# Kernel optimization log

Measured on AMD Instinct MI355X. Metric: run time of the kernel, lower is better.

## Reference

```python
import jax, jax.numpy as jnp
import numpy as np

N_NODES = 100000
N_GRAPHS = 64
EPS = 1e-5


def _sage_conv(x, src, dst, Wl, bl, Wr):
    # mean-aggregate neighbor messages (src -> dst), then lin_l(agg) + lin_r(x)
    n = x.shape[0]
    deg = jax.ops.segment_sum(jnp.ones_like(dst, dtype=x.dtype), dst, num_segments=n)
    agg = jax.ops.segment_sum(x[src], dst, num_segments=n)  # [N, d]
    agg = agg / jnp.maximum(deg, 1.0)[:, None]
    return agg @ Wl + bl + x @ Wr


def _bn_relu(x, gamma, beta):
    mu = jnp.mean(x, axis=0)
    var = jnp.var(x, axis=0)
    return jax.nn.relu((x - mu) * jax.lax.rsqrt(var + EPS) * gamma + beta)


def setup_inputs() -> dict:
    key = jax.random.key(0)
    ks = jax.random.split(key, 16)
    E = 1600000
    x = jax.random.normal(ks[0], (N_NODES, 2), dtype=jnp.float32)
    edge_index = jax.random.randint(ks[1], (2, E), 0, N_NODES, dtype=jnp.int64)
    batch = jnp.sort(jax.random.randint(ks[2], (N_NODES,), 0, N_GRAPHS, dtype=jnp.int64))

    def lin(k, din, dout):
        s = 1.0 / np.sqrt(din)
        return jax.random.uniform(k, (din, dout), jnp.float32, -s, s)

    d = {"x": x, "edge_index": edge_index, "batch": batch}
    dims = [(2, 32), (32, 64), (64, 128)]
    for i, (din, dout) in enumerate(dims, 1):
        k1, k2 = jax.random.split(ks[2 + i])
        d[f"Wl{i}"] = lin(k1, din, dout)
        d[f"bl{i}"] = jnp.zeros((dout,), jnp.float32)
        d[f"Wr{i}"] = lin(k2, din, dout)
        d[f"g{i}"] = jnp.ones((dout,), jnp.float32)
        d[f"be{i}"] = jnp.zeros((dout,), jnp.float32)
    d["Wf1"] = lin(ks[10], 128, 64)
    d["bf1"] = jnp.zeros((64,), jnp.float32)
    d["Wf2"] = lin(ks[11], 64, 1)
    d["bf2"] = jnp.zeros((1,), jnp.float32)
    return d


def reference(x, edge_index, batch,
              Wl1, bl1, Wr1, g1, be1,
              Wl2, bl2, Wr2, g2, be2,
              Wl3, bl3, Wr3, g3, be3,
              Wf1, bf1, Wf2, bf2):
    src, dst = edge_index[0], edge_index[1]
    h = _bn_relu(_sage_conv(x, src, dst, Wl1, bl1, Wr1), g1, be1)
    h = _bn_relu(_sage_conv(h, src, dst, Wl2, bl2, Wr2), g2, be2)
    h = _bn_relu(_sage_conv(h, src, dst, Wl3, bl3, Wr3), g3, be3)
    # global mean pool over graphs
    cnt = jax.ops.segment_sum(jnp.ones_like(batch, dtype=h.dtype), batch, num_segments=N_GRAPHS)
    pooled = jax.ops.segment_sum(h, batch, num_segments=N_GRAPHS) / jnp.maximum(cnt, 1.0)[:, None]
    out = jax.nn.relu(pooled @ Wf1 + bf1)
    # dropout is identity in eval mode
    return out @ Wf2 + bf2
```

## Files before the change

### kernel.cpp

```cpp
#include <hip/hip_runtime.h>
#include <hip/hip_fp16.h>

#define N_NODES 100000
#define N_GRAPHS 64
#define BN_EPS 1e-5

#define NB 782
#define NC 49
#define PT1 4096
#define PT2 2048
#define BPC 16
#define CAP 3072
#define CAPC 36864
#define CAPF 3072

typedef _Float16 f16x8 __attribute__((ext_vector_type(8)));
typedef float f32x4 __attribute__((ext_vector_type(4)));

union F16x8u {
    f16x8 v;
    __half2 h2[4];
    uint4 u;
};

__device__ __forceinline__ float bfly64(float v) {
#pragma unroll
    for (int m = 1; m < 64; m <<= 1) v += __shfl_xor(v, m, 64);
    return v;
}

__device__ __forceinline__ unsigned pack_h2(float a, float b) {
    __half2 h = __floats2half2_rn(a, b);
    unsigned w;
    __builtin_memcpy(&w, &h, 4);
    return w;
}

__device__ __forceinline__ float2 unpack_h2(unsigned w) {
    __half2 h;
    __builtin_memcpy(&h, &w, 4);
    return __half22float2(h);
}

__global__ void cur_init(int* __restrict__ ccur, int* __restrict__ fcur) {
    int t = threadIdx.x;
    if (t < NC) ccur[t] = t * CAPC;
    if (t < 784) fcur[t] = t * CAPF;
}

__global__ __launch_bounds__(256)
void part1(const int* __restrict__ dst, const int* __restrict__ src,
           int* __restrict__ ccur, int* __restrict__ cdst, int* __restrict__ csrc, int E) {
    __shared__ int ld[PT1], ls[PT1];
    __shared__ unsigned char lb[PT1];
    __shared__ int hist[NC], lbase[NC], gbase[NC];
    long long t0 = (long long)blockIdx.x * PT1;
    int n = (int)min((long long)PT1, (long long)E - t0);
    int tid = threadIdx.x;
    for (int i = tid; i < NC; i += 256) hist[i] = 0;
    __syncthreads();
    int d[PT1 / 256], s[PT1 / 256], c[PT1 / 256];
#pragma unroll
    for (int k = 0; k < PT1 / 256; ++k) {
        int li = k * 256 + tid;
        if (li < n) {
            d[k] = __builtin_nontemporal_load(dst + t0 + li);
            s[k] = __builtin_nontemporal_load(src + t0 + li);
            c[k] = d[k] >> 11;
            atomicAdd(&hist[c[k]], 1);
        }
    }
    __syncthreads();
    if (tid == 0) {
        int run = 0;
        for (int i = 0; i < NC; ++i) { lbase[i] = run; run += hist[i]; }
    }
    __syncthreads();
    if (tid < NC) gbase[tid] = atomicAdd(&ccur[tid], hist[tid]);
    __syncthreads();
    for (int i = tid; i < NC; i += 256) hist[i] = 0;
    __syncthreads();
#pragma unroll
    for (int k = 0; k < PT1 / 256; ++k) {
        int li = k * 256 + tid;
        if (li < n) {
            int pos = lbase[c[k]] + atomicAdd(&hist[c[k]], 1);
            ld[pos] = d[k]; ls[pos] = s[k]; lb[pos] = (unsigned char)c[k];
        }
    }
    __syncthreads();
    for (int i = tid; i < n; i += 256) {
        int bb = lb[i];
        int g = gbase[bb] + (i - lbase[bb]);
        cdst[g] = ld[i];
        csrc[g] = ls[i];
    }
}

__global__ __launch_bounds__(256)
void part2(const int* __restrict__ cdst, const int* __restrict__ csrc,
           const int* __restrict__ ccur, int* __restrict__ fcur,
           int* __restrict__ qdst, int* __restrict__ qsrc) {
    __shared__ int ld[PT2], ls[PT2];
    __shared__ unsigned char lb[PT2];
    __shared__ int hist[16], lbase[16], gbase[16];
    int c = blockIdx.x / BPC;
    int j = blockIdx.x % BPC;
    int beg = c * CAPC;
    int end = ccur[c];
    int tid = threadIdx.x;
    for (int t0 = beg + j * PT2; t0 < end; t0 += BPC * PT2) {
        int n = min(PT2, end - t0);
        if (tid < 16) hist[tid] = 0;
        __syncthreads();
        int d[PT2 / 256], s[PT2 / 256], f[PT2 / 256];
#pragma unroll
        for (int k = 0; k < PT2 / 256; ++k) {
            int li = k * 256 + tid;
            if (li < n) {
                d[k] = cdst[t0 + li];
                s[k] = csrc[t0 + li];
                f[k] = (d[k] >> 7) & 15;
                atomicAdd(&hist[f[k]], 1);
            }
        }
        __syncthreads();
        if (tid == 0) {
            int run = 0;
            for (int i = 0; i < 16; ++i) { lbase[i] = run; run += hist[i]; }
        }
        __syncthreads();
        if (tid < 16) gbase[tid] = atomicAdd(&fcur[(c << 4) + tid], hist[tid]);
        __syncthreads();
        if (tid < 16) hist[tid] = 0;
        __syncthreads();
#pragma unroll
        for (int k = 0; k < PT2 / 256; ++k) {
            int li = k * 256 + tid;
            if (li < n) {
                int pos = lbase[f[k]] + atomicAdd(&hist[f[k]], 1);
                ld[pos] = d[k]; ls[pos] = s[k]; lb[pos] = (unsigned char)f[k];
            }
        }
        __syncthreads();
        for (int i = tid; i < n; i += 256) {
            int bb = lb[i];
            int g = gbase[bb] + (i - lbase[bb]);
            qdst[g] = ld[i];
            qsrc[g] = ls[i];
        }
        __syncthreads();
    }
}

__global__ __launch_bounds__(256)
void fill_final(const int* __restrict__ qdst, const int* __restrict__ qsrc,
                const int* __restrict__ fcur, int* __restrict__ offs,
                int* __restrict__ oend, int* __restrict__ nbr, int N) {
    __shared__ int cnt[128], cbase[128], cur[128];
    __shared__ int lout[CAP];
    int b = blockIdx.x;
    int nlo = b << 7;
    int nn = min(128, N - nlo);
    int ebeg = b * CAPF;
    int ne = fcur[b] - ebeg;
    int tid = threadIdx.x;
    if (tid < 128) { cnt[tid] = 0; cur[tid] = 0; }
    __syncthreads();
    for (int i = tid; i < ne; i += 256)
        atomicAdd(&cnt[qdst[ebeg + i] - nlo], 1);
    __syncthreads();
    if (tid < 128) cbase[tid] = cnt[tid];
    __syncthreads();
    for (int st = 1; st < 128; st <<= 1) {
        int v = 0;
        if (tid < 128 && tid >= st) v = cbase[tid - st];
        __syncthreads();
        if (tid < 128 && tid >= st) cbase[tid] += v;
        __syncthreads();
    }
    if (tid < nn) {
        offs[nlo + tid] = ebeg + (tid ? cbase[tid - 1] : 0);
        oend[nlo + tid] = ebeg + cbase[tid];
    }
    __syncthreads();
    for (int i = tid; i < ne; i += 256) {
        int d = qdst[ebeg + i];
        int s = qsrc[ebeg + i];
        int ln = d - nlo;
        int p = (ln ? cbase[ln - 1] : 0) + atomicAdd(&cur[ln], 1);
        lout[p] = s;
    }
    __syncthreads();
    for (int i = tid; i < ne; i += 256)
        nbr[ebeg + i] = lout[i];
}

__global__ __launch_bounds__(256)
void layer1_fused(const float2* __restrict__ x2,
                  const int* __restrict__ offs, const int* __restrict__ oend,
                  const int* __restrict__ nbr,
                  const float* __restrict__ Wl, const float* __restrict__ bl,
                  const float* __restrict__ Wr,
                  __half* __restrict__ hout16,
                  double* __restrict__ sums, int N) {
    __shared__ float sAr[64];
    int tid = threadIdx.x;
    if (tid < 64) sAr[tid] = 0.f;
    __syncthreads();
    int n = blockIdx.x * 256 + tid;
    bool valid = (n < N);
    int beg = 0, end = 0;
    if (valid) { beg = offs[n]; end = oend[n]; }
    float ax0 = 0.f, ay0 = 0.f, ax1 = 0.f, ay1 = 0.f;
    int j = beg;
    for (; j + 16 <= end; j += 16) {
        int s[16];
#pragma unroll
        for (int u = 0; u < 16; ++u) s[u] = __builtin_nontemporal_load(nbr + j + u);
        float2 v[16];
#pragma unroll
        for (int u = 0; u < 16; ++u) v[u] = x2[s[u]];
#pragma unroll
        for (int u = 0; u < 16; ++u) {
            if (u & 1) { ax1 += v[u].x; ay1 += v[u].y; }
            else       { ax0 += v[u].x; ay0 += v[u].y; }
        }
    }
    for (; j + 4 <= end; j += 4) {
        int s[4];
#pragma unroll
        for (int u = 0; u < 4; ++u) s[u] = __builtin_nontemporal_load(nbr + j + u);
        float2 v[4];
#pragma unroll
        for (int u = 0; u < 4; ++u) v[u] = x2[s[u]];
        ax0 += v[0].x; ay0 += v[0].y;
        ax1 += v[1].x; ay1 += v[1].y;
        ax0 += v[2].x; ay0 += v[2].y;
        ax1 += v[3].x; ay1 += v[3].y;
    }
    for (; j < end; ++j) {
        float2 v = x2[nbr[j]];
        ax0 += v.x; ay0 += v.y;
    }
    float invd = 1.0f / fmaxf((float)(end - beg), 1.0f);
    float a0 = (ax0 + ax1) * invd, a1 = (ay0 + ay1) * invd;
    float x0 = 0.f, x1 = 0.f;
    if (valid) {
        float2 xv = x2[n];
        x0 = xv.x; x1 = xv.y;
    }
    float acc[32];
#pragma unroll
    for (int jj = 0; jj < 32; ++jj)
        acc[jj] = bl[jj] + a0 * Wl[jj] + a1 * Wl[32 + jj] + x0 * Wr[jj] + x1 * Wr[32 + jj];
    if (valid) {
        unsigned w[16];
#pragma unroll
        for (int p = 0; p < 16; ++p) w[p] = pack_h2(acc[2*p], acc[2*p+1]);
        uint4* q = (uint4*)(hout16 + (size_t)n * 32);
        q[0] = make_uint4(w[0], w[1], w[2], w[3]);
        q[1] = make_uint4(w[4], w[5], w[6], w[7]);
        q[2] = make_uint4(w[8], w[9], w[10], w[11]);
        q[3] = make_uint4(w[12], w[13], w[14], w[15]);
    }
    int lane = tid & 63;
#pragma unroll
    for (int jj = 0; jj < 32; ++jj) {
        float v = valid ? acc[jj] : 0.f;
        float s = bfly64(v);
        float q = bfly64(v * v);
        if (lane == jj) atomicAdd(&sAr[jj], s);
        if (lane == 32 + jj) atomicAdd(&sAr[32 + jj], q);
    }
    __syncthreads();
    if (tid < 64) atomicAdd(&sums[tid], (double)sAr[tid]);
}

template<int F>
__global__ __launch_bounds__(256)
void bn_apply(const uint4* __restrict__ h, const double* __restrict__ sums,
              const float* __restrict__ gamma, const float* __restrict__ beta,
              uint4* __restrict__ out, int N) {
    __shared__ __align__(16) float lsc[F], lsf[F];
    int tid = threadIdx.x;
    if (tid < F) {
        double mu = sums[tid] / (double)N_NODES;
        double var = sums[F + tid] / (double)N_NODES - mu * mu;
        if (var < 0.0) var = 0.0;
        double sc = (double)gamma[tid] / sqrt(var + BN_EPS);
        lsc[tid] = (float)sc;
        lsf[tid] = (float)((double)beta[tid] - mu * sc);
    }
    __syncthreads();
    constexpr int FV = F / 8;
    int total = N * FV;
    for (int i = blockIdx.x * 256 + tid; i < total; i += gridDim.x * 256) {
        uint4 v = h[i];
        int c4 = (i & (FV - 1)) * 2;
        float4 sca = ((const float4*)lsc)[c4];
        float4 scb = ((const float4*)lsc)[c4 + 1];
        float4 sfa = ((const float4*)lsf)[c4];
        float4 sfb = ((const float4*)lsf)[c4 + 1];
        float2 f0 = unpack_h2(v.x), f1 = unpack_h2(v.y);
        float2 f2 = unpack_h2(v.z), f3 = unpack_h2(v.w);
        uint4 o;
        o.x = pack_h2(fmaxf(f0.x * sca.x + sfa.x, 0.f), fmaxf(f0.y * sca.y + sfa.y, 0.f));
        o.y = pack_h2(fmaxf(f1.x * sca.z + sfa.z, 0.f), fmaxf(f1.y * sca.w + sfa.w, 0.f));
        o.z = pack_h2(fmaxf(f2.x * scb.x + sfb.x, 0.f), fmaxf(f2.y * scb.y + sfb.y, 0.f));
        o.w = pack_h2(fmaxf(f3.x * scb.z + sfb.z, 0.f), fmaxf(f3.y * scb.w + sfb.w, 0.f));
        out[i] = o;
    }
}

__device__ __forceinline__ void accum8_h16(float* acc, uint4 v) {
    float2 f0 = unpack_h2(v.x), f1 = unpack_h2(v.y);
    float2 f2 = unpack_h2(v.z), f3 = unpack_h2(v.w);
    acc[0] += f0.x; acc[1] += f0.y; acc[2] += f1.x; acc[3] += f1.y;
    acc[4] += f2.x; acc[5] += f2.y; acc[6] += f3.x; acc[7] += f3.y;
}

template<int F>
__global__ __launch_bounds__(256)
void agg_sum(const uint4* __restrict__ xb, const int* __restrict__ offs,
             const int* __restrict__ oend, const int* __restrict__ nbr,
             uint4* __restrict__ aggh, int N) {
    constexpr int FV = F / 8;
    constexpr int NPB = 256 / FV;
    int n = blockIdx.x * NPB + threadIdx.y;
    if (n >= N) return;
    int f = threadIdx.x;
    int beg = offs[n], end = oend[n];
    float a0[8], a1[8];
#pragma unroll
    for (int q = 0; q < 8; ++q) { a0[q] = 0.f; a1[q] = 0.f; }
    int j = beg;
    for (; j + 16 <= end; j += 16) {
        int s[16];
#pragma unroll
        for (int u = 0; u < 16; ++u) s[u] = __builtin_nontemporal_load(nbr + j + u);
        uint4 v[16];
#pragma unroll
        for (int u = 0; u < 16; ++u) v[u] = xb[s[u] * FV + f];
#pragma unroll
        for (int u = 0; u < 16; ++u)
            accum8_h16((u & 1) ? a1 : a0, v[u]);
    }
    if (j + 8 <= end) {
        int s[8];
#pragma unroll
        for (int u = 0; u < 8; ++u) s[u] = __builtin_nontemporal_load(nbr + j + u);
        uint4 v[8];
#pragma unroll
        for (int u = 0; u < 8; ++u) v[u] = xb[s[u] * FV + f];
#pragma unroll
        for (int u = 0; u < 8; ++u)
            accum8_h16((u & 1) ? a1 : a0, v[u]);
        j += 8;
    }
    if (j + 4 <= end) {
        int s[4];
#pragma unroll
        for (int u = 0; u < 4; ++u) s[u] = __builtin_nontemporal_load(nbr + j + u);
        uint4 v[4];
#pragma unroll
        for (int u = 0; u < 4; ++u) v[u] = xb[s[u] * FV + f];
#pragma unroll
        for (int u = 0; u < 4; ++u)
            accum8_h16((u & 1) ? a1 : a0, v[u]);
        j += 4;
    }
    for (; j < end; ++j) {
        uint4 v = xb[__builtin_nontemporal_load(nbr + j) * FV + f];
        accum8_h16(a0, v);
    }
    float invd = 1.0f / fmaxf((float)(end - beg), 1.0f);
    uint4 o;
    o.x = pack_h2((a0[0] + a1[0]) * invd, (a0[1] + a1[1]) * invd);
    o.y = pack_h2((a0[2] + a1[2]) * invd, (a0[3] + a1[3]) * invd);
    o.z = pack_h2((a0[4] + a1[4]) * invd, (a0[5] + a1[5]) * invd);
    o.w = pack_h2((a0[6] + a1[6]) * invd, (a0[7] + a1[7]) * invd);
    aggh[n * FV + f] = o;
}

__global__ __launch_bounds__(256)
void pack_w(const float* __restrict__ Wl2, const float* __restrict__ Wr2,
            const float* __restrict__ Wl3, const float* __restrict__ Wr3,
            __half* __restrict__ pk) {
    int e = blockIdx.x * 256 + threadIdx.x;
    const float* W; int le, DOUT, NCB, base, SZ;
    if (e < 2048)       { W = Wl2; le = e;         DOUT = 64;  NCB = 4; base = 0;     SZ = 2048; }
    else if (e < 4096)  { W = Wr2; le = e - 2048;  DOUT = 64;  NCB = 4; base = 4096;  SZ = 2048; }
    else if (e < 12288) { W = Wl3; le = e - 4096;  DOUT = 128; NCB = 8; base = 8192;  SZ = 8192; }
    else                { W = Wr3; le = e - 12288; DOUT = 128; NCB = 8; base = 24576; SZ = 8192; }
    int i = le & 7;
    int lane = (le >> 3) & 63;
    int cbkb = le >> 9;
    int cb = cbkb % NCB;
    int kb = cbkb / NCB;
    int k = kb * 32 + ((lane >> 4) << 3) + i;
    int col = cb * 16 + (lane & 15);
    float w = W[k * DOUT + col];
    __half h = __float2half(w);
    float lo = w - __half2float(h);
    pk[base + le] = h;
    pk[base + SZ + le] = __float2half(lo);
}

template<int DIN, int DOUT>
__global__ __launch_bounds__(256)
void linear_mfma(const __half* __restrict__ bnx16, const __half* __restrict__ agg16,
                 const __half* __restrict__ wlhi, const __half* __restrict__ wllo,
                 const __half* __restrict__ wrhi, const __half* __restrict__ wrlo,
                 const float* __restrict__ bl,
                 __half* __restrict__ hout16, float* __restrict__ partial, int N) {
    constexpr int KB = DIN / 32;
    constexpr int NCB = DOUT / 16;
    constexpr int MREP = 2;
    constexpr int MB = 4 * MREP * 16;
    __shared__ float blkS[DOUT], blkQ[DOUT];
    int tid = threadIdx.x;
    for (int i = tid; i < DOUT; i += 256) { blkS[i] = 0.f; blkQ[i] = 0.f; }
    __syncthreads();
    int n0 = blockIdx.x * MB;

    int wave = tid >> 6;
    int lane = tid & 63;
    int rlane = lane & 15;
    int kg = lane >> 4;
    int rbase = n0 + wave * (MREP * 16);

    f16x8 aA[MREP][KB], aX[MREP][KB];
#pragma unroll
    for (int m = 0; m < MREP; ++m) {
        int row = rbase + m * 16 + rlane;
        int rowc = min(row, N - 1);
#pragma unroll
        for (int kb = 0; kb < KB; ++kb) {
            int c0 = kb * 32 + kg * 8;
            F16x8u ta, tx;
            ta.u = *(const uint4*)(agg16 + (size_t)rowc * DIN + c0);
            tx.u = *(const uint4*)(bnx16 + (size_t)rowc * DIN + c0);
            aA[m][kb] = ta.v;
            aX[m][kb] = tx.v;
        }
    }

    f32x4 acc[MREP][NCB];
#pragma unroll
    for (int cb = 0; cb < NCB; ++cb) {
        float bv = bl[cb * 16 + rlane];
#pragma unroll
        for (int m = 0; m < MREP; ++m)
            acc[m][cb] = {bv, bv, bv, bv};
    }

#pragma unroll
    for (int cb = 0; cb < NCB; ++cb) {
#pragma unroll
        for (int kb = 0; kb < KB; ++kb) {
            size_t fo = ((size_t)(kb * NCB + cb) * 64 + lane) * 8;
            f16x8 blh = *(const f16x8*)(wlhi + fo);
            f16x8 bll = *(const f16x8*)(wllo + fo);
            f16x8 brh = *(const f16x8*)(wrhi + fo);
            f16x8 brl = *(const f16x8*)(wrlo + fo);
#pragma unroll
            for (int m = 0; m < MREP; ++m) {
                acc[m][cb] = __builtin_amdgcn_mfma_f32_16x16x32_f16(aA[m][kb], blh, acc[m][cb], 0, 0, 0);
                acc[m][cb] = __builtin_amdgcn_mfma_f32_16x16x32_f16(aA[m][kb], bll, acc[m][cb], 0, 0, 0);
                acc[m][cb] = __builtin_amdgcn_mfma_f32_16x16x32_f16(aX[m][kb], brh, acc[m][cb], 0, 0, 0);
                acc[m][cb] = __builtin_amdgcn_mfma_f32_16x16x32_f16(aX[m][kb], brl, acc[m][cb], 0, 0, 0);
            }
        }
    }

#pragma unroll
    for (int m = 0; m < MREP; ++m) {
        int rowb = rbase + m * 16 + kg * 4;
#pragma unroll
        for (int r = 0; r < 4; ++r) {
            int node = rowb + r;
            if (node < N) {
#pragma unroll
                for (int cb = 0; cb < NCB; ++cb)
                    hout16[(size_t)node * DOUT + cb * 16 + rlane] = __float2half(acc[m][cb][r]);
            }
        }
    }

#pragma unroll
    for (int cb = 0; cb < NCB; ++cb) {
        float s = 0.f, q = 0.f;
#pragma unroll
        for (int m = 0; m < MREP; ++m) {
            int rowb = rbase + m * 16 + kg * 4;
#pragma unroll
            for (int r = 0; r < 4; ++r) {
                if (rowb + r < N) {
                    float v = acc[m][cb][r];
                    s += v; q += v * v;
                }
            }
        }
        s += __shfl_xor(s, 16, 64); s += __shfl_xor(s, 32, 64);
        q += __shfl_xor(q, 16, 64); q += __shfl_xor(q, 32, 64);
        if (kg == 0) {
            atomicAdd(&blkS[cb * 16 + rlane], s);
            atomicAdd(&blkQ[cb * 16 + rlane], q);
        }
    }
    __syncthreads();
    float* po = partial + (size_t)blockIdx.x * (2 * DOUT);
    for (int i = tid; i < DOUT; i += 256) {
        po[i] = blkS[i];
        po[DOUT + i] = blkQ[i];
    }
}

template<int F>
__global__ __launch_bounds__(256)
void stats_finalize2(const float* __restrict__ partial, double* __restrict__ sums, int P) {
    __shared__ double sh[256];
    int i = blockIdx.x;
    int t = threadIdx.x;
    double a = 0.0;
    for (int k = t; k < P; k += 256)
        a += (double)partial[(size_t)k * (2 * F) + i];
    sh[t] = a;
    __syncthreads();
    for (int st = 128; st > 0; st >>= 1) {
        if (t < st) sh[t] += sh[t + st];
        __syncthreads();
    }
    if (t == 0) sums[i] = sh[0];
}

__global__ void pool_partial(const __half* __restrict__ h, const int* __restrict__ batch,
                             const double* __restrict__ sums,
                             const float* __restrict__ gamma, const float* __restrict__ beta,
                             double* __restrict__ pooled_d, int N) {
    __shared__ float lsc[128], lsf[128];
    const int CH = 64;
    int f = threadIdx.x;
    {
        double mu = sums[f] / (double)N_NODES;
        double var = sums[128 + f] / (double)N_NODES - mu * mu;
        if (var < 0.0) var = 0.0;
        double sc = (double)gamma[f] / sqrt(var + BN_EPS);
        lsc[f] = (float)sc;
        lsf[f] = (float)((double)beta[f] - mu * sc);
    }
    __syncthreads();
    int n0 = blockIdx.x * CH;
    if (n0 >= N) return;
    int n1 = min(n0 + CH, N);
    float sc = lsc[f], sf = lsf[f];
    int g = batch[n0];
    float acc = 0.f;
    for (int n = n0; n < n1; ++n) {
        int bg = batch[n];
        if (bg != g) {
            atomicAdd(&pooled_d[g * 128 + f], (double)acc);
            acc = 0.f;
            g = bg;
        }
        float v = __half2float(h[(long long)n * 128 + f]);
        acc += fmaxf(v * sc + sf, 0.f);
    }
    atomicAdd(&pooled_d[g * 128 + f], (double)acc);
}

__global__ void mlp_fused(const double* __restrict__ pooled_d, const int* __restrict__ batch,
                          const float* __restrict__ Wf1, const float* __restrict__ bf1,
                          const float* __restrict__ Wf2, const float* __restrict__ bf2,
                          float* __restrict__ out, int N) {
    __shared__ float sp[128];
    int g = blockIdx.x;
    int t = threadIdx.x;
    int lo = 0, hi = N;
    while (lo < hi) { int m = (lo + hi) >> 1; if (batch[m] < g) lo = m + 1; else hi = m; }
    int start = lo;
    hi = N;
    while (lo < hi) { int m = (lo + hi) >> 1; if (batch[m] < g + 1) lo = m + 1; else hi = m; }
    int cnt = lo - start;
    sp[t] = (float)(pooled_d[g * 128 + t] / (double)max(cnt, 1));
    __syncthreads();
    if (t < 64) {
        float hacc = bf1[t];
#pragma unroll 8
        for (int k = 0; k < 128; ++k) hacc += sp[k] * Wf1[k * 64 + t];
        hacc = fmaxf(hacc, 0.f) * Wf2[t];
        for (int o = 32; o > 0; o >>= 1) hacc += __shfl_down(hacc, o);
        if (t == 0) out[g] = hacc + bf2[0];
    }
}

extern "C" void kernel_launch(void* const* d_in, const int* in_sizes, int n_in,
                              void* d_out, int out_size, void* d_ws, size_t ws_size,
                              hipStream_t stream) {
    const float* x     = (const float*)d_in[0];
    const int*   ei    = (const int*)d_in[1];
    const int*   batch = (const int*)d_in[2];
    const float *Wl1=(const float*)d_in[3],  *bl1=(const float*)d_in[4],  *Wr1=(const float*)d_in[5];
    const float *g1 =(const float*)d_in[6],  *be1=(const float*)d_in[7];
    const float *Wl2=(const float*)d_in[8],  *bl2=(const float*)d_in[9],  *Wr2=(const float*)d_in[10];
    const float *g2 =(const float*)d_in[11], *be2=(const float*)d_in[12];
    const float *Wl3=(const float*)d_in[13], *bl3=(const float*)d_in[14], *Wr3=(const float*)d_in[15];
    const float *g3 =(const float*)d_in[16], *be3=(const float*)d_in[17];
    const float *Wf1=(const float*)d_in[18], *bf1=(const float*)d_in[19];
    const float *Wf2=(const float*)d_in[20], *bf2=(const float*)d_in[21];

    const int N = N_NODES;
    const int E = in_sizes[1] / 2;
    const int* src = ei;
    const int* dst = ei + E;

    char* ws = (char*)d_ws;
    size_t off = 0;
    auto salloc = [&](size_t bytes) {
        void* p = ws + off;
        off += (bytes + 255) & ~(size_t)255;
        return p;
    };
    double* sums    = (double*)salloc(768 * 8);
    double* pooledd = (double*)salloc((size_t)N_GRAPHS * 128 * 8);
    size_t zero_bytes = off;
    int*    offs    = (int*)   salloc((size_t)N * 4);
    int*    oend    = (int*)   salloc((size_t)N * 4);
    int*    fcur    = (int*)   salloc(784 * 4);
    int*    ccur    = (int*)   salloc(NC * 4);
    int*    nbr     = (int*)   salloc((size_t)NB * CAPF * 4);
    float*  partial = (float*) salloc((size_t)1024 * 256 * 4);
    __half* pk      = (__half*)salloc((size_t)40960 * 2);
    __half* h1h     = (__half*)salloc((size_t)(N + 256) * 32 * 2);
    __half* b1h     = (__half*)salloc((size_t)(N + 256) * 32 * 2);
    __half* h2h     = (__half*)salloc((size_t)(N + 256) * 64 * 2);
    __half* b2h     = (__half*)salloc((size_t)(N + 256) * 64 * 2);
    __half* h3h     = (__half*)salloc((size_t)(N + 256) * 128 * 2);
    __half* aggh    = (__half*)salloc((size_t)(N + 256) * 64 * 2);
    (void)ws_size;

    double* sums1 = sums, *sums2 = sums + 256, *sums3 = sums + 512;
    int* cdst = (int*)h3h;
    int* csrc = cdst + (size_t)NC * CAPC;
    int* qdst = (int*)aggh;
    int* qsrc = (int*)h2h;

    const __half *pwl2h = pk,         *pwl2l = pk + 2048;
    const __half *pwr2h = pk + 4096,  *pwr2l = pk + 6144;
    const __half *pwl3h = pk + 8192,  *pwl3l = pk + 16384;
    const __half *pwr3h = pk + 24576, *pwr3l = pk + 32768;

    hipMemsetAsync(sums, 0, zero_bytes, stream);

    pack_w<<<80, 256, 0, stream>>>(Wl2, Wr2, Wl3, Wr3, pk);
    cur_init<<<1, 1024, 0, stream>>>(ccur, fcur);

    part1<<<(E + PT1 - 1) / PT1, 256, 0, stream>>>(dst, src, ccur, cdst, csrc, E);
    part2<<<NC * BPC, 256, 0, stream>>>(cdst, csrc, ccur, fcur, qdst, qsrc);
    fill_final<<<NB, 256, 0, stream>>>(qdst, qsrc, fcur, offs, oend, nbr, N);

    const int NL = (N + 255) / 256;
    const int NBLK = (N + 127) / 128;

    layer1_fused<<<NL, 256, 0, stream>>>((const float2*)x, offs, oend, nbr,
                                          Wl1, bl1, Wr1, h1h, sums1, N);

    bn_apply<32><<<512, 256, 0, stream>>>((const uint4*)h1h, sums1, g1, be1, (uint4*)b1h, N);
    agg_sum<32><<<(N + 63) / 64, dim3(4, 64), 0, stream>>>(
        (const uint4*)b1h, offs, oend, nbr, (uint4*)aggh, N);
    linear_mfma<32, 64><<<NBLK, 256, 0, stream>>>(
        b1h, (const __half*)aggh, pwl2h, pwl2l, pwr2h, pwr2l, bl2, h2h, partial, N);
    stats_finalize2<64><<<128, 256, 0, stream>>>(partial, sums2, NBLK);

    bn_apply<64><<<512, 256, 0, stream>>>((const uint4*)h2h, sums2, g2, be2, (uint4*)b2h, N);
    agg_sum<64><<<(N + 31) / 32, dim3(8, 32), 0, stream>>>(
        (const uint4*)b2h, offs, oend, nbr, (uint4*)aggh, N);
    linear_mfma<64, 128><<<NBLK, 256, 0, stream>>>(
        b2h, (const __half*)aggh, pwl3h, pwl3l, pwr3h, pwr3l, bl3, h3h, partial, N);
    stats_finalize2<128><<<256, 256, 0, stream>>>(partial, sums3, NBLK);

    pool_partial<<<(N + 63) / 64, 128, 0, stream>>>(h3h, batch, sums3, g3, be3, pooledd, N);
    mlp_fused<<<N_GRAPHS, 128, 0, stream>>>(pooledd, batch, Wf1, bf1, Wf2, bf2, (float*)d_out, N);
}
```

Before: 312.4 us.

## Pack dst low bits and src into one int for edge partition passes

After: 307.4 us. Within noise of the previous version (-1.6%).

```diff
diff --git a/kernel.cpp b/kernel.cpp
--- a/kernel.cpp
+++ b/kernel.cpp
@@ -42,16 +42,40 @@
     return __half22float2(h);
 }
 
-__global__ void cur_init(int* __restrict__ ccur, int* __restrict__ fcur) {
-    int t = threadIdx.x;
-    if (t < NC) ccur[t] = t * CAPC;
-    if (t < 784) fcur[t] = t * CAPF;
-}
+__global__ __launch_bounds__(256)
+void pack_w(const float* __restrict__ Wl2, const float* __restrict__ Wr2,
+            const float* __restrict__ Wl3, const float* __restrict__ Wr3,
+            __half* __restrict__ pk, int* __restrict__ ccur, int* __restrict__ fcur) {
+    int tid = threadIdx.x;
+    if (blockIdx.x == 0) {
+        for (int t = tid; t < NC; t += 256) ccur[t] = t * CAPC;
+        for (int t = tid; t < 784; t += 256) fcur[t] = t * CAPF;
+    }
+    int e = blockIdx.x * 256 + tid;
+    const float* W; int le, DOUT, NCB, base, SZ;
+    if (e < 2048)       { W = Wl2; le = e;         DOUT = 64;  NCB = 4; base = 0;     SZ = 2048; }
+    else if (e < 4096)  { W = Wr2; le = e - 2048;  DOUT = 64;  NCB = 4; base = 4096;  SZ = 2048; }
+    else if (e < 12288) { W = Wl3; le = e - 4096;  DOUT = 128; NCB = 8; base = 8192;  SZ = 8192; }
+    else                { W = Wr3; le = e - 12288; DOUT = 128; NCB = 8; base = 24576; SZ = 8192; }
+    int i = le & 7;
+    int lane = (le >> 3) & 63;
+    int cbkb = le >> 9;
+    int cb = cbkb % NCB;
+    int kb = cbkb / NCB;
+    int k = kb * 32 + ((lane >> 4) << 3) + i;
+    int col = cb * 16 + (lane & 15);
+    float w = W[k * DOUT + col];
+    __half h = __float2half(w);
+    float lo = w - __half2float(h);
+    pk[base + le] = h;
+    pk[base + SZ + le] = __float2half(lo);
+}
+
 
 __global__ __launch_bounds__(256)
 void part1(const int* __restrict__ dst, const int* __restrict__ src,
-           int* __restrict__ ccur, int* __restrict__ cdst, int* __restrict__ csrc, int E) {
-    __shared__ int ld[PT1], ls[PT1];
+           int* __restrict__ ccur, int* __restrict__ cpk, int E) {
+    __shared__ int ld[PT1];
     __shared__ unsigned char lb[PT1];
     __shared__ int hist[NC], lbase[NC], gbase[NC];
     long long t0 = (long long)blockIdx.x * PT1;
@@ -59,14 +83,15 @@
     int tid = threadIdx.x;
     for (int i = tid; i < NC; i += 256) hist[i] = 0;
     __syncthreads();
-    int d[PT1 / 256], s[PT1 / 256], c[PT1 / 256];
+    int p[PT1 / 256], c[PT1 / 256];
 #pragma unroll
     for (int k = 0; k < PT1 / 256; ++k) {
         int li = k * 256 + tid;
         if (li < n) {
-            d[k] = __builtin_nontemporal_load(dst + t0 + li);
-            s[k] = __builtin_nontemporal_load(src + t0 + li);
-            c[k] = d[k] >> 11;
+            int d = __builtin_nontemporal_load(dst + t0 + li);
+            int s = __builtin_nontemporal_load(src + t0 + li);
+            c[k] = d >> 11;
+            p[k] = ((d & 2047) << 17) | s;
             atomicAdd(&hist[c[k]], 1);
         }
     }
@@ -85,23 +110,21 @@
         int li = k * 256 + tid;
         if (li < n) {
             int pos = lbase[c[k]] + atomicAdd(&hist[c[k]], 1);
-            ld[pos] = d[k]; ls[pos] = s[k]; lb[pos] = (unsigned char)c[k];
+            ld[pos] = p[k]; lb[pos] = (unsigned char)c[k];
         }
     }
     __syncthreads();
     for (int i = tid; i < n; i += 256) {
         int bb = lb[i];
         int g = gbase[bb] + (i - lbase[bb]);
-        cdst[g] = ld[i];
-        csrc[g] = ls[i];
-    }
-}
-
-__global__ __launch_bounds__(256)
-void part2(const int* __restrict__ cdst, const int* __restrict__ csrc,
-           const int* __restrict__ ccur, int* __restrict__ fcur,
-           int* __restrict__ qdst, int* __restrict__ qsrc) {
-    __shared__ int ld[PT2], ls[PT2];
+        cpk[g] = ld[i];
+    }
+}
+
+__global__ __launch_bounds__(256)
+void part2(const int* __restrict__ cpk, const int* __restrict__ ccur,
+           int* __restrict__ fcur, int* __restrict__ qpk) {
+    __shared__ int ld[PT2];
     __shared__ unsigned char lb[PT2];
     __shared__ int hist[16], lbase[16], gbase[16];
     int c = blockIdx.x / BPC;
@@ -113,14 +136,13 @@
         int n = min(PT2, end - t0);
         if (tid < 16) hist[tid] = 0;
         __syncthreads();
-        int d[PT2 / 256], s[PT2 / 256], f[PT2 / 256];
+        int p[PT2 / 256], f[PT2 / 256];
 #pragma unroll
         for (int k = 0; k < PT2 / 256; ++k) {
             int li = k * 256 + tid;
             if (li < n) {
-                d[k] = cdst[t0 + li];
-                s[k] = csrc[t0 + li];
-                f[k] = (d[k] >> 7) & 15;
+                p[k] = cpk[t0 + li];
+                f[k] = (p[k] >> 24) & 15;
                 atomicAdd(&hist[f[k]], 1);
             }
         }
@@ -139,24 +161,23 @@
             int li = k * 256 + tid;
             if (li < n) {
                 int pos = lbase[f[k]] + atomicAdd(&hist[f[k]], 1);
-                ld[pos] = d[k]; ls[pos] = s[k]; lb[pos] = (unsigned char)f[k];
+                ld[pos] = p[k]; lb[pos] = (unsigned char)f[k];
             }
         }
         __syncthreads();
         for (int i = tid; i < n; i += 256) {
             int bb = lb[i];
             int g = gbase[bb] + (i - lbase[bb]);
-            qdst[g] = ld[i];
-            qsrc[g] = ls[i];
-        }
-        __syncthreads();
-    }
-}
-
-__global__ __launch_bounds__(256)
-void fill_final(const int* __restrict__ qdst, const int* __restrict__ qsrc,
-                const int* __restrict__ fcur, int* __restrict__ offs,
-                int* __restrict__ oend, int* __restrict__ nbr, int N) {
+            qpk[g] = ld[i];
+        }
+        __syncthreads();
+    }
+}
+
+__global__ __launch_bounds__(256)
+void fill_final(const int* __restrict__ qpk, const int* __restrict__ fcur,
+                int* __restrict__ offs, int* __restrict__ oend,
+                int* __restrict__ nbr, int N) {
     __shared__ int cnt[128], cbase[128], cur[128];
     __shared__ int lout[CAP];
     int b = blockIdx.x;
@@ -168,7 +189,7 @@
     if (tid < 128) { cnt[tid] = 0; cur[tid] = 0; }
     __syncthreads();
     for (int i = tid; i < ne; i += 256)
-        atomicAdd(&cnt[qdst[ebeg + i] - nlo], 1);
+        atomicAdd(&cnt[(qpk[ebeg + i] >> 17) & 127], 1);
     __syncthreads();
     if (tid < 128) cbase[tid] = cnt[tid];
     __syncthreads();
@@ -185,11 +206,10 @@
     }
     __syncthreads();
     for (int i = tid; i < ne; i += 256) {
-        int d = qdst[ebeg + i];
-        int s = qsrc[ebeg + i];
-        int ln = d - nlo;
-        int p = (ln ? cbase[ln - 1] : 0) + atomicAdd(&cur[ln], 1);
-        lout[p] = s;
+        int p = qpk[ebeg + i];
+        int ln = (p >> 17) & 127;
+        int pos = (ln ? cbase[ln - 1] : 0) + atomicAdd(&cur[ln], 1);
+        lout[pos] = p & 0x1FFFF;
     }
     __syncthreads();
     for (int i = tid; i < ne; i += 256)
@@ -381,30 +401,6 @@
     o.z = pack_h2((a0[4] + a1[4]) * invd, (a0[5] + a1[5]) * invd);
     o.w = pack_h2((a0[6] + a1[6]) * invd, (a0[7] + a1[7]) * invd);
     aggh[n * FV + f] = o;
-}
-
-__global__ __launch_bounds__(256)
-void pack_w(const float* __restrict__ Wl2, const float* __restrict__ Wr2,
-            const float* __restrict__ Wl3, const float* __restrict__ Wr3,
-            __half* __restrict__ pk) {
-    int e = blockIdx.x * 256 + threadIdx.x;
-    const float* W; int le, DOUT, NCB, base, SZ;
-    if (e < 2048)       { W = Wl2; le = e;         DOUT = 64;  NCB = 4; base = 0;     SZ = 2048; }
-    else if (e < 4096)  { W = Wr2; le = e - 2048;  DOUT = 64;  NCB = 4; base = 4096;  SZ = 2048; }
-    else if (e < 12288) { W = Wl3; le = e - 4096;  DOUT = 128; NCB = 8; base = 8192;  SZ = 8192; }
-    else                { W = Wr3; le = e - 12288; DOUT = 128; NCB = 8; base = 24576; SZ = 8192; }
-    int i = le & 7;
-    int lane = (le >> 3) & 63;
-    int cbkb = le >> 9;
-    int cb = cbkb % NCB;
-    int kb = cbkb / NCB;
-    int k = kb * 32 + ((lane >> 4) << 3) + i;
-    int col = cb * 16 + (lane & 15);
-    float w = W[k * DOUT + col];
-    __half h = __float2half(w);
-    float lo = w - __half2float(h);
-    pk[base + le] = h;
-    pk[base + SZ + le] = __float2half(lo);
 }
 
 template<int DIN, int DOUT>
@@ -641,10 +637,8 @@
     (void)ws_size;
 
     double* sums1 = sums, *sums2 = sums + 256, *sums3 = sums + 512;
-    int* cdst = (int*)h3h;
-    int* csrc = cdst + (size_t)NC * CAPC;
-    int* qdst = (int*)aggh;
-    int* qsrc = (int*)h2h;
+    int* cpk = (int*)h3h;
+    int* qpk = (int*)aggh;
 
     const __half *pwl2h = pk,         *pwl2l = pk + 2048;
     const __half *pwr2h = pk + 4096,  *pwr2l = pk + 6144;
@@ -653,12 +647,11 @@
 
     hipMemsetAsync(sums, 0, zero_bytes, stream);
 
-    pack_w<<<80, 256, 0, stream>>>(Wl2, Wr2, Wl3, Wr3, pk);
-    cur_init<<<1, 1024, 0, stream>>>(ccur, fcur);
-
-    part1<<<(E + PT1 - 1) / PT1, 256, 0, stream>>>(dst, src, ccur, cdst, csrc, E);
-    part2<<<NC * BPC, 256, 0, stream>>>(cdst, csrc, ccur, fcur, qdst, qsrc);
-    fill_final<<<NB, 256, 0, stream>>>(qdst, qsrc, fcur, offs, oend, nbr, N);
+    pack_w<<<80, 256, 0, stream>>>(Wl2, Wr2, Wl3, Wr3, pk, ccur, fcur);
+
+    part1<<<(E + PT1 - 1) / PT1, 256, 0, stream>>>(dst, src, ccur, cpk, E);
+    part2<<<NC * BPC, 256, 0, stream>>>(cpk, ccur, fcur, qpk);
+    fill_final<<<NB, 256, 0, stream>>>(qpk, fcur, offs, oend, nbr, N);
 
     const int NL = (N + 255) / 256;
     const int NBLK = (N + 127) / 128;
```
